# Optimization experiments

Hardware: AMD Instinct MI355X
Metric: run time of the kernel (lower is better)

## Reference

```python
import jax, jax.numpy as jnp
import numpy as np

TEMPERATURE = 12.5   # args.temperature (DeepEMD default)
EPS = 0.05           # entropic regularization for the OT (EMD) solve
N_ITERS = 100        # Sinkhorn iterations
COS_EPS = 1e-8       # F.cosine_similarity eps


def setup_inputs() -> dict:
    key = jax.random.key(0)
    k1, k2 = jax.random.split(key)
    B, C, H, W = 512, 1024, 8, 8
    proto = jax.random.normal(k1, (B, C, H, W), dtype=jnp.float32)
    query = jax.random.normal(k2, (B, C, H, W), dtype=jnp.float32)
    return {"proto": proto, "query": query}


def get_weight_vector(A, Bmap):
    """A,[b,c,h,w]; pooled Bmap reweights A's channels -> node weights [b, h*w]."""
    pooled = Bmap.mean(axis=(2, 3), keepdims=True)          # adaptive_avg_pool2d -> [b,c,1,1]
    comb = (A * pooled).sum(axis=1).reshape(A.shape[0], -1)  # [b, h*w]
    return jax.nn.relu(comb) + 0.001


def center(x):
    # args.norm == 'center': subtract channel mean
    return x - x.mean(axis=1, keepdims=True)


def cosine_sim_map(proto, query):
    """sim[b, q_node, p_node] = cosine similarity between flattened spatial nodes."""
    B, C = proto.shape[0], proto.shape[1]
    p = proto.reshape(B, C, -1).transpose(0, 2, 1)   # [b, Np, c]
    q = query.reshape(B, C, -1).transpose(0, 2, 1)   # [b, Nq, c]
    pn = p / jnp.maximum(jnp.linalg.norm(p, axis=-1, keepdims=True), COS_EPS)
    qn = q / jnp.maximum(jnp.linalg.norm(q, axis=-1, keepdims=True), COS_EPS)
    return jnp.einsum('bqc,bpc->bqp', qn, pn)        # [b, Nq, Np]


def sinkhorn_flow(cost, r, c):
    """Entropic-regularized OT flow with marginals r [b,N], c [b,M]; cost [b,N,M]."""
    K = jnp.exp(-cost / EPS)
    v0 = jnp.ones_like(c)

    def body(v, _):
        u = r / jnp.maximum(jnp.einsum('bnm,bm->bn', K, v), 1e-30)
        v = c / jnp.maximum(jnp.einsum('bnm,bn->bm', K, u), 1e-30)
        return v, None

    v, _ = jax.lax.scan(body, v0, None, length=N_ITERS)
    u = r / jnp.maximum(jnp.einsum('bnm,bm->bn', K, v), 1e-30)
    return u[:, :, None] * K * v[:, None, :]         # [b, N, M]


def reference(proto, query):
    # emd_forward(proto, query)
    weight_1 = get_weight_vector(query, proto)       # [b, Nq]
    weight_2 = get_weight_vector(proto, query)       # [b, Np]
    p = center(proto)
    q = center(query)
    sim = cosine_sim_map(p, q)                       # [b, Nq, Np]
    # get_emd_distance: solve OT on cost = 1 - sim with (normalized) node weights
    r = weight_1 / weight_1.sum(axis=-1, keepdims=True)
    c = weight_2 / weight_2.sum(axis=-1, keepdims=True)
    flow = sinkhorn_flow(1.0 - sim, r, c)
    num_node = weight_1.shape[-1]
    logits = (sim * flow).sum(axis=(-1, -2)) * (TEMPERATURE / num_node)
    return logits
```

## Files before the change

### kernel.cpp

```cpp
#include <hip/hip_runtime.h>
#include <math.h>

#define NCH    1024
#define NN     64
#define CK     32
#define KSC    28.853900817779268f
#define SPLIT  4
#define WSB    4352

#define STAT_Q(v) { sqp[0]+=(v).x; q2p[0]=fmaf((v).x,(v).x,q2p[0]); \
                    sqp[1]+=(v).y; q2p[1]=fmaf((v).y,(v).y,q2p[1]); \
                    sqp[2]+=(v).z; q2p[2]=fmaf((v).z,(v).z,q2p[2]); \
                    sqp[3]+=(v).w; q2p[3]=fmaf((v).w,(v).w,q2p[3]); }
#define STAT_P(v) { spp[0]+=(v).x; p2p[0]=fmaf((v).x,(v).x,p2p[0]); \
                    spp[1]+=(v).y; p2p[1]=fmaf((v).y,(v).y,p2p[1]); \
                    spp[2]+=(v).z; p2p[2]=fmaf((v).z,(v).z,p2p[2]); \
                    spp[3]+=(v).w; p2p[3]=fmaf((v).w,(v).w,p2p[3]); }

#define GRAM_CHUNK_BODY(NCHUNK_, QB_, PB_)                                     \
    for (int ch = 0; ch < (NCHUNK_); ++ch) {                                   \
        if (ch) __syncthreads();                                               \
        *(float4*)&stage[       ofs] = qv0;                                    \
        *(float4*)&stage[1024 + ofs] = qv1;                                    \
        *(float4*)&stage[2048 + ofs] = pv0;                                    \
        *(float4*)&stage[3072 + ofs] = pv1;                                    \
        float4 nq0, nq1, np0, np1;                                             \
        const bool more = (ch + 1 < (NCHUNK_));                                \
        if (more) {                                                            \
            const float* qn = (QB_) + (ch + 1) * 2048;                         \
            const float* pn = (PB_) + (ch + 1) * 2048;                         \
            nq0 = *(const float4*)(qn + ofs);                                  \
            nq1 = *(const float4*)(qn + 1024 + ofs);                           \
            np0 = *(const float4*)(pn + ofs);                                  \
            np1 = *(const float4*)(pn + 1024 + ofs);                           \
        }                                                                      \
        STAT_Q(qv0); STAT_Q(qv1);                                              \
        STAT_P(pv0); STAT_P(pv1);                                              \
        __syncthreads();                                                       \
        _Pragma("unroll 8")                                                    \
        for (int cc = 0; cc < CK; ++cc) {                                      \
            float4 a  = *(const float4*)&stage[cc * 64 + n0];                  \
            float4 bb = *(const float4*)&stage[2048 + cc * 64 + m0];           \
            acc[0][0]=fmaf(a.x,bb.x,acc[0][0]); acc[0][1]=fmaf(a.x,bb.y,acc[0][1]); \
            acc[0][2]=fmaf(a.x,bb.z,acc[0][2]); acc[0][3]=fmaf(a.x,bb.w,acc[0][3]); \
            acc[1][0]=fmaf(a.y,bb.x,acc[1][0]); acc[1][1]=fmaf(a.y,bb.y,acc[1][1]); \
            acc[1][2]=fmaf(a.y,bb.z,acc[1][2]); acc[1][3]=fmaf(a.y,bb.w,acc[1][3]); \
            acc[2][0]=fmaf(a.z,bb.x,acc[2][0]); acc[2][1]=fmaf(a.z,bb.y,acc[2][1]); \
            acc[2][2]=fmaf(a.z,bb.z,acc[2][2]); acc[2][3]=fmaf(a.z,bb.w,acc[2][3]); \
            acc[3][0]=fmaf(a.w,bb.x,acc[3][0]); acc[3][1]=fmaf(a.w,bb.y,acc[3][1]); \
            acc[3][2]=fmaf(a.w,bb.z,acc[3][2]); acc[3][3]=fmaf(a.w,bb.w,acc[3][3]); \
        }                                                                      \
        if (more) { qv0 = nq0; qv1 = nq1; pv0 = np0; pv1 = np1; }              \
    }

#define DOT16(KK, ARR) ({ \
    float4 x0 = *(const float4*)&ARR[sp4*16 +  0]; \
    float4 x1 = *(const float4*)&ARR[sp4*16 +  4]; \
    float4 x2 = *(const float4*)&ARR[sp4*16 +  8]; \
    float4 x3 = *(const float4*)&ARR[sp4*16 + 12]; \
    float a0 = 0.0f, a1 = 0.0f; \
    a0=fmaf(KK[0],x0.x,a0);  a1=fmaf(KK[1],x0.y,a1); \
    a0=fmaf(KK[2],x0.z,a0);  a1=fmaf(KK[3],x0.w,a1); \
    a0=fmaf(KK[4],x1.x,a0);  a1=fmaf(KK[5],x1.y,a1); \
    a0=fmaf(KK[6],x1.z,a0);  a1=fmaf(KK[7],x1.w,a1); \
    a0=fmaf(KK[8],x2.x,a0);  a1=fmaf(KK[9],x2.y,a1); \
    a0=fmaf(KK[10],x2.z,a0); a1=fmaf(KK[11],x2.w,a1); \
    a0=fmaf(KK[12],x3.x,a0); a1=fmaf(KK[13],x3.y,a1); \
    a0=fmaf(KK[14],x3.z,a0); a1=fmaf(KK[15],x3.w,a1); \
    a0 + a1; })

__global__ __launch_bounds__(256)
void gram_partial(const float* __restrict__ proto,
                  const float* __restrict__ query,
                  float* __restrict__ ws)
{
    __shared__ __align__(16) float stage[4096];

    const int bid = blockIdx.x;
    const int b = bid >> 2, s = bid & (SPLIT - 1);
    const int t  = threadIdx.x;
    const int tr = t >> 4, tc = t & 15;
    const int n0 = tr * 4, m0 = tc * 4;
    const int ofs = 4 * t;

    const float* __restrict__ pb = proto + (size_t)b * (NCH * NN) + s * (NCH / SPLIT) * NN;
    const float* __restrict__ qb = query + (size_t)b * (NCH * NN) + s * (NCH / SPLIT) * NN;

    float acc[4][4];
    #pragma unroll
    for (int i = 0; i < 4; ++i)
        #pragma unroll
        for (int j = 0; j < 4; ++j) acc[i][j] = 0.0f;
    float sqp[4] = {0,0,0,0}, q2p[4] = {0,0,0,0};
    float spp[4] = {0,0,0,0}, p2p[4] = {0,0,0,0};

    float4 qv0 = *(const float4*)(qb + ofs);
    float4 qv1 = *(const float4*)(qb + 1024 + ofs);
    float4 pv0 = *(const float4*)(pb + ofs);
    float4 pv1 = *(const float4*)(pb + 1024 + ofs);

    GRAM_CHUNK_BODY(NCH / SPLIT / CK, qb, pb)
    __syncthreads();

    float* __restrict__ wsb = ws + (size_t)bid * WSB;
    #pragma unroll
    for (int i = 0; i < 4; ++i) {
        float4 v; v.x = acc[i][0]; v.y = acc[i][1]; v.z = acc[i][2]; v.w = acc[i][3];
        *(float4*)&wsb[(n0 + i) * 64 + m0] = v;
    }

    #pragma unroll
    for (int k = 0; k < 4; ++k) {
        stage[t*16 +      k] = sqp[k];
        stage[t*16 +  4 + k] = q2p[k];
        stage[t*16 +  8 + k] = spp[k];
        stage[t*16 + 12 + k] = p2p[k];
    }
    __syncthreads();
    if (t < NN) {
        const int g = t >> 2, k = t & 3;
        float ssq = 0, sq2 = 0, ssp = 0, sp2 = 0;
        #pragma unroll
        for (int j = 0; j < 16; ++j) {
            const float* row = &stage[(j * 16 + g) * 16];
            ssq += row[k]; sq2 += row[4 + k]; ssp += row[8 + k]; sp2 += row[12 + k];
        }
        wsb[4096 +   0 + t] = ssq;
        wsb[4096 +  64 + t] = sq2;
        wsb[4096 + 128 + t] = ssp;
        wsb[4096 + 192 + t] = sp2;
    }
}

__global__ __launch_bounds__(256)
void emd_solve(const float* __restrict__ ws, float* __restrict__ out)
{
    __shared__ __align__(16) float stage[16 * 64];
    __shared__ __align__(16) float Kl [NN][68];
    __shared__ __align__(16) float KTl[NN][68];
    __shared__ __align__(16) float statL[4][NN];
    __shared__ __align__(16) float uL[NN];
    __shared__ __align__(16) float vL[NN];
    __shared__ __align__(16) float rL[NN];
    __shared__ __align__(16) float cL[NN];
    __shared__ float redl[4];

    const int b  = blockIdx.x;
    const int t  = threadIdx.x;
    const int tr = t >> 4, tc = t & 15;
    const int n0 = tr * 4, m0 = tc * 4;

    const float* __restrict__ wsb = ws + (size_t)b * SPLIT * WSB;

    float acc[4][4];
    #pragma unroll
    for (int i = 0; i < 4; ++i)
        #pragma unroll
        for (int j = 0; j < 4; ++j) acc[i][j] = 0.0f;
    #pragma unroll
    for (int s = 0; s < SPLIT; ++s) {
        const float* __restrict__ g = wsb + s * WSB;
        #pragma unroll
        for (int i = 0; i < 4; ++i) {
            float4 v = *(const float4*)&g[(n0 + i) * 64 + m0];
            acc[i][0] += v.x; acc[i][1] += v.y; acc[i][2] += v.z; acc[i][3] += v.w;
        }
    }
    if (t < NN) {
        float s0 = 0, s1 = 0, s2 = 0, s3 = 0;
        #pragma unroll
        for (int s = 0; s < SPLIT; ++s) {
            const float* __restrict__ g = wsb + s * WSB + 4096;
            s0 += g[t]; s1 += g[64 + t]; s2 += g[128 + t]; s3 += g[192 + t];
        }
        statL[0][t] = s0; statL[1][t] = s1; statL[2][t] = s2; statL[3][t] = s3;
    }
    #pragma unroll
    for (int i = 0; i < 4; ++i) {
        float s = acc[i][0] + acc[i][1] + acc[i][2] + acc[i][3];
        s += __shfl_xor(s, 1, 64); s += __shfl_xor(s, 2, 64);
        s += __shfl_xor(s, 4, 64); s += __shfl_xor(s, 8, 64);
        if (tc == 0) uL[n0 + i] = s;
    }
    #pragma unroll
    for (int j = 0; j < 4; ++j)
        stage[tr * 64 + m0 + j] = acc[0][j] + acc[1][j] + acc[2][j] + acc[3][j];
    __syncthreads();

    if (t < NN) {
        float cs = 0;
        #pragma unroll
        for (int i = 0; i < 16; ++i) cs += stage[i * 64 + t];
        float w2 = fmaxf(cs * (1.0f/64.0f), 0.0f) + 0.001f;
        float w1 = fmaxf(uL[t] * (1.0f/64.0f), 0.0f) + 0.001f;
        float s1 = w1, s2 = w2;
        #pragma unroll
        for (int m = 1; m < 64; m <<= 1) {
            s1 += __shfl_xor(s1, m, 64);
            s2 += __shfl_xor(s2, m, 64);
        }
        rL[t] = w1 / s1;
        cL[t] = w2 / s2;
        vL[t] = 1.0f;
    }
    {
        float nq_[4], np_[4], sqn[4], spm[4];
        #pragma unroll
        for (int i = 0; i < 4; ++i) {
            float sv  = statL[0][n0 + i];
            float var = statL[1][n0 + i] - sv * sv * (1.0f/1024.0f);
            nq_[i] = fmaxf(sqrtf(fmaxf(var, 0.0f)), 1e-8f);
            sqn[i] = sv;
        }
        #pragma unroll
        for (int j = 0; j < 4; ++j) {
            float sv  = statL[2][m0 + j];
            float var = statL[3][m0 + j] - sv * sv * (1.0f/1024.0f);
            np_[j] = fmaxf(sqrtf(fmaxf(var, 0.0f)), 1e-8f);
            spm[j] = sv;
        }
        #pragma unroll
        for (int i = 0; i < 4; ++i) {
            #pragma unroll
            for (int j = 0; j < 4; ++j) {
                float sim = (acc[i][j] - sqn[i] * spm[j] * (1.0f/1024.0f)) / (nq_[i] * np_[j]);
                acc[i][j] = sim;
                float Kv = exp2f((sim - 1.0f) * KSC);
                Kl [n0 + i][m0 + j] = Kv;
                KTl[m0 + j][n0 + i] = Kv;
            }
        }
    }
    __syncthreads();

    const int sn  = t >> 2;
    const int sp4 = t & 3;
    float Kr[16], KTr[16];
    #pragma unroll
    for (int jj = 0; jj < 4; ++jj) {
        float4 kv = *(const float4*)&Kl [sn][sp4 * 16 + jj * 4];
        float4 kt = *(const float4*)&KTl[sn][sp4 * 16 + jj * 4];
        Kr [jj*4+0]=kv.x; Kr [jj*4+1]=kv.y; Kr [jj*4+2]=kv.z; Kr [jj*4+3]=kv.w;
        KTr[jj*4+0]=kt.x; KTr[jj*4+1]=kt.y; KTr[jj*4+2]=kt.z; KTr[jj*4+3]=kt.w;
    }
    const float rreg = rL[sn];
    const float creg = cL[sn];

    for (int it = 0; it < 100; ++it) {
        float s = DOT16(Kr, vL);
        s += __shfl_xor(s, 1, 64); s += __shfl_xor(s, 2, 64);
        float u = rreg / fmaxf(s, 1e-30f);
        if (sp4 == 0) uL[sn] = u;
        __syncthreads();
        float s2 = DOT16(KTr, uL);
        s2 += __shfl_xor(s2, 1, 64); s2 += __shfl_xor(s2, 2, 64);
        float vv = creg / fmaxf(s2, 1e-30f);
        if (sp4 == 0) vL[sn] = vv;
        __syncthreads();
    }
    {
        float s = DOT16(Kr, vL);
        s += __shfl_xor(s, 1, 64); s += __shfl_xor(s, 2, 64);
        float u = rreg / fmaxf(s, 1e-30f);
        if (sp4 == 0) uL[sn] = u;
    }
    __syncthreads();

    float uu[4], vv_[4];
    #pragma unroll
    for (int i = 0; i < 4; ++i) uu[i]  = uL[n0 + i];
    #pragma unroll
    for (int j = 0; j < 4; ++j) vv_[j] = vL[m0 + j];
    float part = 0.0f;
    #pragma unroll
    for (int i = 0; i < 4; ++i) {
        #pragma unroll
        for (int j = 0; j < 4; ++j) {
            float sim = acc[i][j];
            float Kv  = exp2f((sim - 1.0f) * KSC);
            part = fmaf(sim * Kv, uu[i] * vv_[j], part);
        }
    }
    #pragma unroll
    for (int m = 1; m < 64; m <<= 1) part += __shfl_xor(part, m, 64);
    if ((t & 63) == 0) redl[t >> 6] = part;
    __syncthreads();
    if (t == 0) out[b] = (redl[0] + redl[1] + redl[2] + redl[3]) * (12.5f / 64.0f);
}

__global__ __launch_bounds__(256)
void deepemd_fused(const float* __restrict__ proto,
                   const float* __restrict__ query,
                   float* __restrict__ out)
{
    __shared__ __align__(16) float stage[2 * CK * NN];
    __shared__ __align__(16) float Kl [NN][68];
    __shared__ __align__(16) float KTl[NN][68];
    __shared__ __align__(16) float statL[4][NN];
    __shared__ __align__(16) float uL[NN];
    __shared__ __align__(16) float vL[NN];
    __shared__ __align__(16) float rL[NN];
    __shared__ __align__(16) float cL[NN];
    __shared__ float redl[4];

    const int b  = blockIdx.x;
    const int t  = threadIdx.x;
    const int tr = t >> 4, tc = t & 15;
    const int n0 = tr * 4, m0 = tc * 4;
    const int ofs = 4 * t;

    const float* __restrict__ pb = proto + (size_t)b * (NCH * NN);
    const float* __restrict__ qb = query + (size_t)b * (NCH * NN);

    float acc[4][4];
    #pragma unroll
    for (int i = 0; i < 4; ++i)
        #pragma unroll
        for (int j = 0; j < 4; ++j) acc[i][j] = 0.0f;
    float sqp[4] = {0,0,0,0}, q2p[4] = {0,0,0,0};
    float spp[4] = {0,0,0,0}, p2p[4] = {0,0,0,0};

    float4 qv0 = *(const float4*)(qb + ofs);
    float4 qv1 = *(const float4*)(qb + 1024 + ofs);
    float4 pv0 = *(const float4*)(pb + ofs);
    float4 pv1 = *(const float4*)(pb + 1024 + ofs);

    GRAM_CHUNK_BODY(NCH / CK, qb, pb)
    __syncthreads();

    #pragma unroll
    for (int i = 0; i < 4; ++i) {
        float s = acc[i][0] + acc[i][1] + acc[i][2] + acc[i][3];
        s += __shfl_xor(s, 1, 64); s += __shfl_xor(s, 2, 64);
        s += __shfl_xor(s, 4, 64); s += __shfl_xor(s, 8, 64);
        if (tc == 0) uL[n0 + i] = s;
    }
    #pragma unroll
    for (int k = 0; k < 4; ++k) {
        stage[t*16 +      k] = sqp[k];
        stage[t*16 +  4 + k] = q2p[k];
        stage[t*16 +  8 + k] = spp[k];
        stage[t*16 + 12 + k] = p2p[k];
    }
    __syncthreads();
    if (t < NN) {
        const int g = t >> 2, k = t & 3;
        float ssq = 0, sq2 = 0, ssp = 0, sp2 = 0;
        #pragma unroll
        for (int j = 0; j < 16; ++j) {
            const float* row = &stage[(j * 16 + g) * 16];
            ssq += row[k]; sq2 += row[4 + k]; ssp += row[8 + k]; sp2 += row[12 + k];
        }
        statL[0][t] = ssq; statL[1][t] = sq2; statL[2][t] = ssp; statL[3][t] = sp2;
    }
    __syncthreads();
    #pragma unroll
    for (int j = 0; j < 4; ++j)
        stage[tr * 64 + m0 + j] = acc[0][j] + acc[1][j] + acc[2][j] + acc[3][j];
    __syncthreads();
    if (t < NN) {
        float cs = 0;
        #pragma unroll
        for (int i = 0; i < 16; ++i) cs += stage[i * 64 + t];
        float w2 = fmaxf(cs * (1.0f/64.0f), 0.0f) + 0.001f;
        float w1 = fmaxf(uL[t] * (1.0f/64.0f), 0.0f) + 0.001f;
        float s1 = w1, s2 = w2;
        #pragma unroll
        for (int m = 1; m < 64; m <<= 1) {
            s1 += __shfl_xor(s1, m, 64);
            s2 += __shfl_xor(s2, m, 64);
        }
        rL[t] = w1 / s1;
        cL[t] = w2 / s2;
        vL[t] = 1.0f;
    }
    __syncthreads();

    {
        float nq_[4], np_[4], sqn[4], spm[4];
        #pragma unroll
        for (int i = 0; i < 4; ++i) {
            float sv  = statL[0][n0 + i];
            float var = statL[1][n0 + i] - sv * sv * (1.0f/1024.0f);
            nq_[i] = fmaxf(sqrtf(fmaxf(var, 0.0f)), 1e-8f);
            sqn[i] = sv;
        }
        #pragma unroll
        for (int j = 0; j < 4; ++j) {
            float sv  = statL[2][m0 + j];
            float var = statL[3][m0 + j] - sv * sv * (1.0f/1024.0f);
            np_[j] = fmaxf(sqrtf(fmaxf(var, 0.0f)), 1e-8f);
            spm[j] = sv;
        }
        #pragma unroll
        for (int i = 0; i < 4; ++i) {
            #pragma unroll
            for (int j = 0; j < 4; ++j) {
                float sim = (acc[i][j] - sqn[i] * spm[j] * (1.0f/1024.0f)) / (nq_[i] * np_[j]);
                acc[i][j] = sim;
                float Kv = exp2f((sim - 1.0f) * KSC);
                Kl [n0 + i][m0 + j] = Kv;
                KTl[m0 + j][n0 + i] = Kv;
            }
        }
    }
    __syncthreads();

    const int sn  = t >> 2;
    const int sp4 = t & 3;
    float Kr[16], KTr[16];
    #pragma unroll
    for (int jj = 0; jj < 4; ++jj) {
        float4 kv = *(const float4*)&Kl [sn][sp4 * 16 + jj * 4];
        float4 kt = *(const float4*)&KTl[sn][sp4 * 16 + jj * 4];
        Kr [jj*4+0]=kv.x; Kr [jj*4+1]=kv.y; Kr [jj*4+2]=kv.z; Kr [jj*4+3]=kv.w;
        KTr[jj*4+0]=kt.x; KTr[jj*4+1]=kt.y; KTr[jj*4+2]=kt.z; KTr[jj*4+3]=kt.w;
    }
    const float rreg = rL[sn];
    const float creg = cL[sn];

    for (int it = 0; it < 100; ++it) {
        float s = DOT16(Kr, vL);
        s += __shfl_xor(s, 1, 64); s += __shfl_xor(s, 2, 64);
        float u = rreg / fmaxf(s, 1e-30f);
        if (sp4 == 0) uL[sn] = u;
        __syncthreads();
        float s2 = DOT16(KTr, uL);
        s2 += __shfl_xor(s2, 1, 64); s2 += __shfl_xor(s2, 2, 64);
        float vv = creg / fmaxf(s2, 1e-30f);
        if (sp4 == 0) vL[sn] = vv;
        __syncthreads();
    }
    {
        float s = DOT16(Kr, vL);
        s += __shfl_xor(s, 1, 64); s += __shfl_xor(s, 2, 64);
        float u = rreg / fmaxf(s, 1e-30f);
        if (sp4 == 0) uL[sn] = u;
    }
    __syncthreads();

    float uu[4], vv_[4];
    #pragma unroll
    for (int i = 0; i < 4; ++i) uu[i]  = uL[n0 + i];
    #pragma unroll
    for (int j = 0; j < 4; ++j) vv_[j] = vL[m0 + j];
    float part = 0.0f;
    #pragma unroll
    for (int i = 0; i < 4; ++i) {
        #pragma unroll
        for (int j = 0; j < 4; ++j) {
            float sim = acc[i][j];
            float Kv  = exp2f((sim - 1.0f) * KSC);
            part = fmaf(sim * Kv, uu[i] * vv_[j], part);
        }
    }
    #pragma unroll
    for (int m = 1; m < 64; m <<= 1) part += __shfl_xor(part, m, 64);
    if ((t & 63) == 0) redl[t >> 6] = part;
    __syncthreads();
    if (t == 0) out[b] = (redl[0] + redl[1] + redl[2] + redl[3]) * (12.5f / 64.0f);
}

extern "C" void kernel_launch(void* const* d_in, const int* in_sizes, int n_in,
                              void* d_out, int out_size, void* d_ws, size_t ws_size,
                              hipStream_t stream) {
    const float* proto = (const float*)d_in[0];
    const float* query = (const float*)d_in[1];
    float* out = (float*)d_out;
    (void)in_sizes; (void)n_in; (void)out_size;

    const size_t need = (size_t)512 * SPLIT * WSB * sizeof(float);
    if (ws_size >= need) {
        gram_partial<<<dim3(512 * SPLIT), dim3(256), 0, stream>>>(proto, query, (float*)d_ws);
        emd_solve  <<<dim3(512),         dim3(256), 0, stream>>>((const float*)d_ws, out);
    } else {
        deepemd_fused<<<dim3(512), dim3(256), 0, stream>>>(proto, query, out);
    }
}
```

Before: 134.5 us.

## Replace LDS-staged Gram kernel with register-blocked per-wave 8x8 tiles

The Gram partial kernel is rewritten so each wave reads its own 128-channel slice straight from global memory into registers, using a four-slot software prefetch, and computes an 8x8 register tile per lane with no LDS staging or per-chunk barriers. Partial Grams from the four waves are then reduced through LDS. The channel split drops from 4 to 2 blocks per batch, which halves workspace traffic and the reduction work in emd_solve. The cost is a 64-float accumulator per thread plus prefetch registers, so register pressure rises and occupancy may drop. Each lane also issues uncoalesced float4 loads of row fragments.

```diff
diff --git a/kernel.cpp b/kernel.cpp
--- a/kernel.cpp
+++ b/kernel.cpp
@@ -5,8 +5,306 @@
 #define NN     64
 #define CK     32
 #define KSC    28.853900817779268f
-#define SPLIT  4
+#define SPLIT  2
 #define WSB    4352
+
+__global__ __launch_bounds__(256)
+void gram4(const float* __restrict__ proto,
+           const float* __restrict__ query,
+           float* __restrict__ ws)
+{
+    __shared__ __align__(16) float GA[4096];
+    __shared__ __align__(16) float GB[4096];
+    __shared__ __align__(16) float st4[4 * 4 * NN];
+
+    const int bid = blockIdx.x;
+    const int b = bid >> 1, h = bid & 1;
+    const int t = threadIdx.x;
+    const int w = t >> 6;
+    const int l = t & 63;
+    const int ri = l >> 3;
+    const int ci = l & 7;
+    const int r0 = ri * 8;
+    const int c0 = ci * 4;
+
+    const float* __restrict__ qw = query + (size_t)b * 65536 + (h * 512 + w * 128) * 64;
+    const float* __restrict__ pw = proto + (size_t)b * 65536 + (h * 512 + w * 128) * 64;
+
+    float acc[8][8];
+    #pragma unroll
+    for (int i = 0; i < 8; ++i)
+        #pragma unroll
+        for (int j = 0; j < 8; ++j) acc[i][j] = 0.0f;
+    float sq = 0.0f, q2 = 0.0f, sp = 0.0f, p2 = 0.0f;
+
+    float4 A0[4], A1[4], B0[4], B1[4];
+    float  QS[4], PS[4];
+
+#define LOADSLOT(K, C) do {                                   \
+        const float* qc_ = qw + (C) * 64;                     \
+        const float* pc_ = pw + (C) * 64;                     \
+        A0[K] = *(const float4*)(qc_ + r0);                   \
+        A1[K] = *(const float4*)(qc_ + r0 + 4);               \
+        B0[K] = *(const float4*)(pc_ + c0);                   \
+        B1[K] = *(const float4*)(pc_ + c0 + 32);              \
+        QS[K] = qc_[l];                                       \
+        PS[K] = pc_[l];                                       \
+    } while (0)
+
+#define COMPUTESLOT(K) do {                                   \
+        const float av[8] = {A0[K].x,A0[K].y,A0[K].z,A0[K].w, \
+                             A1[K].x,A1[K].y,A1[K].z,A1[K].w};\
+        const float bv[8] = {B0[K].x,B0[K].y,B0[K].z,B0[K].w, \
+                             B1[K].x,B1[K].y,B1[K].z,B1[K].w};\
+        sq += QS[K]; q2 = fmaf(QS[K], QS[K], q2);             \
+        sp += PS[K]; p2 = fmaf(PS[K], PS[K], p2);             \
+        _Pragma("unroll")                                     \
+        for (int i = 0; i < 8; ++i)                           \
+            _Pragma("unroll")                                 \
+            for (int j = 0; j < 8; ++j)                       \
+                acc[i][j] = fmaf(av[i], bv[j], acc[i][j]);    \
+    } while (0)
+
+    LOADSLOT(0, 0); LOADSLOT(1, 1); LOADSLOT(2, 2); LOADSLOT(3, 3);
+
+    #pragma unroll 1
+    for (int g = 0; g < 31; ++g) {
+        const int c = g * 4;
+        COMPUTESLOT(0); LOADSLOT(0, c + 4);
+        COMPUTESLOT(1); LOADSLOT(1, c + 5);
+        COMPUTESLOT(2); LOADSLOT(2, c + 6);
+        COMPUTESLOT(3); LOADSLOT(3, c + 7);
+    }
+    COMPUTESLOT(0); COMPUTESLOT(1); COMPUTESLOT(2); COMPUTESLOT(3);
+#undef LOADSLOT
+#undef COMPUTESLOT
+
+    st4[(0*4 + w)*NN + l] = sq;
+    st4[(1*4 + w)*NN + l] = q2;
+    st4[(2*4 + w)*NN + l] = sp;
+    st4[(3*4 + w)*NN + l] = p2;
+
+    {
+        float* const GT = (w < 2) ? GA : GB;
+        const bool first = ((w & 1) == 0);
+        if (first) {
+            #pragma unroll
+            for (int i = 0; i < 8; ++i) {
+                float4 v0; v0.x=acc[i][0]; v0.y=acc[i][1]; v0.z=acc[i][2]; v0.w=acc[i][3];
+                float4 v1; v1.x=acc[i][4]; v1.y=acc[i][5]; v1.z=acc[i][6]; v1.w=acc[i][7];
+                *(float4*)&GT[(r0 + i) * 64 + c0]      = v0;
+                *(float4*)&GT[(r0 + i) * 64 + c0 + 32] = v1;
+            }
+        }
+        __syncthreads();
+        if (!first) {
+            #pragma unroll
+            for (int i = 0; i < 8; ++i) {
+                float* g0 = &GT[(r0 + i) * 64 + c0];
+                float* g1 = &GT[(r0 + i) * 64 + c0 + 32];
+                float4 d0 = *(const float4*)g0;
+                float4 d1 = *(const float4*)g1;
+                d0.x+=acc[i][0]; d0.y+=acc[i][1]; d0.z+=acc[i][2]; d0.w+=acc[i][3];
+                d1.x+=acc[i][4]; d1.y+=acc[i][5]; d1.z+=acc[i][6]; d1.w+=acc[i][7];
+                *(float4*)g0 = d0;
+                *(float4*)g1 = d1;
+            }
+        }
+        __syncthreads();
+    }
+
+    float* __restrict__ wsb = ws + (size_t)bid * WSB;
+    {
+        const int base = t * 16;
+        #pragma unroll
+        for (int k = 0; k < 4; ++k) {
+            float4 x = *(const float4*)&GA[base + k * 4];
+            float4 y = *(const float4*)&GB[base + k * 4];
+            x.x+=y.x; x.y+=y.y; x.z+=y.z; x.w+=y.w;
+            *(float4*)&wsb[base + k * 4] = x;
+        }
+    }
+    if (t < NN) {
+        #pragma unroll
+        for (int k = 0; k < 4; ++k) {
+            float s = st4[(k*4 + 0)*NN + t] + st4[(k*4 + 1)*NN + t]
+                    + st4[(k*4 + 2)*NN + t] + st4[(k*4 + 3)*NN + t];
+            wsb[4096 + k * 64 + t] = s;
+        }
+    }
+}
+
+#define DOT16(KK, ARR) ({ \
+    float4 x0 = *(const float4*)&ARR[sp4*16 +  0]; \
+    float4 x1 = *(const float4*)&ARR[sp4*16 +  4]; \
+    float4 x2 = *(const float4*)&ARR[sp4*16 +  8]; \
+    float4 x3 = *(const float4*)&ARR[sp4*16 + 12]; \
+    float a0 = 0.0f, a1 = 0.0f; \
+    a0=fmaf(KK[0],x0.x,a0);  a1=fmaf(KK[1],x0.y,a1); \
+    a0=fmaf(KK[2],x0.z,a0);  a1=fmaf(KK[3],x0.w,a1); \
+    a0=fmaf(KK[4],x1.x,a0);  a1=fmaf(KK[5],x1.y,a1); \
+    a0=fmaf(KK[6],x1.z,a0);  a1=fmaf(KK[7],x1.w,a1); \
+    a0=fmaf(KK[8],x2.x,a0);  a1=fmaf(KK[9],x2.y,a1); \
+    a0=fmaf(KK[10],x2.z,a0); a1=fmaf(KK[11],x2.w,a1); \
+    a0=fmaf(KK[12],x3.x,a0); a1=fmaf(KK[13],x3.y,a1); \
+    a0=fmaf(KK[14],x3.z,a0); a1=fmaf(KK[15],x3.w,a1); \
+    a0 + a1; })
+
+__global__ __launch_bounds__(256)
+void emd_solve(const float* __restrict__ ws, float* __restrict__ out)
+{
+    __shared__ __align__(16) float stage[16 * 64];
+    __shared__ __align__(16) float Kl [NN][68];
+    __shared__ __align__(16) float KTl[NN][68];
+    __shared__ __align__(16) float statL[4][NN];
+    __shared__ __align__(16) float uL[NN];
+    __shared__ __align__(16) float vL[NN];
+    __shared__ __align__(16) float rL[NN];
+    __shared__ __align__(16) float cL[NN];
+    __shared__ float redl[4];
+
+    const int b  = blockIdx.x;
+    const int t  = threadIdx.x;
+    const int tr = t >> 4, tc = t & 15;
+    const int n0 = tr * 4, m0 = tc * 4;
+
+    const float* __restrict__ wsb = ws + (size_t)b * SPLIT * WSB;
+
+    float acc[4][4];
+    #pragma unroll
+    for (int i = 0; i < 4; ++i)
+        #pragma unroll
+        for (int j = 0; j < 4; ++j) acc[i][j] = 0.0f;
+    #pragma unroll
+    for (int s = 0; s < SPLIT; ++s) {
+        const float* __restrict__ g = wsb + s * WSB;
+        #pragma unroll
+        for (int i = 0; i < 4; ++i) {
+            float4 v = *(const float4*)&g[(n0 + i) * 64 + m0];
+            acc[i][0] += v.x; acc[i][1] += v.y; acc[i][2] += v.z; acc[i][3] += v.w;
+        }
+    }
+    if (t < NN) {
+        float s0 = 0, s1 = 0, s2 = 0, s3 = 0;
+        #pragma unroll
+        for (int s = 0; s < SPLIT; ++s) {
+            const float* __restrict__ g = wsb + s * WSB + 4096;
+            s0 += g[t]; s1 += g[64 + t]; s2 += g[128 + t]; s3 += g[192 + t];
+        }
+        statL[0][t] = s0; statL[1][t] = s1; statL[2][t] = s2; statL[3][t] = s3;
+    }
+    #pragma unroll
+    for (int i = 0; i < 4; ++i) {
+        float s = acc[i][0] + acc[i][1] + acc[i][2] + acc[i][3];
+        s += __shfl_xor(s, 1, 64); s += __shfl_xor(s, 2, 64);
+        s += __shfl_xor(s, 4, 64); s += __shfl_xor(s, 8, 64);
+        if (tc == 0) uL[n0 + i] = s;
+    }
+    #pragma unroll
+    for (int j = 0; j < 4; ++j)
+        stage[tr * 64 + m0 + j] = acc[0][j] + acc[1][j] + acc[2][j] + acc[3][j];
+    __syncthreads();
+
+    if (t < NN) {
+        float cs = 0;
+        #pragma unroll
+        for (int i = 0; i < 16; ++i) cs += stage[i * 64 + t];
+        float w2 = fmaxf(cs * (1.0f/64.0f), 0.0f) + 0.001f;
+        float w1 = fmaxf(uL[t] * (1.0f/64.0f), 0.0f) + 0.001f;
+        float s1 = w1, s2 = w2;
+        #pragma unroll
+        for (int m = 1; m < 64; m <<= 1) {
+            s1 += __shfl_xor(s1, m, 64);
+            s2 += __shfl_xor(s2, m, 64);
+        }
+        rL[t] = w1 / s1;
+        cL[t] = w2 / s2;
+        vL[t] = 1.0f;
+    }
+    {
+        float nq_[4], np_[4], sqn[4], spm[4];
+        #pragma unroll
+        for (int i = 0; i < 4; ++i) {
+            float sv  = statL[0][n0 + i];
+            float var = statL[1][n0 + i] - sv * sv * (1.0f/1024.0f);
+            nq_[i] = fmaxf(sqrtf(fmaxf(var, 0.0f)), 1e-8f);
+            sqn[i] = sv;
+        }
+        #pragma unroll
+        for (int j = 0; j < 4; ++j) {
+            float sv  = statL[2][m0 + j];
+            float var = statL[3][m0 + j] - sv * sv * (1.0f/1024.0f);
+            np_[j] = fmaxf(sqrtf(fmaxf(var, 0.0f)), 1e-8f);
+            spm[j] = sv;
+        }
+        #pragma unroll
+        for (int i = 0; i < 4; ++i) {
+            #pragma unroll
+            for (int j = 0; j < 4; ++j) {
+                float sim = (acc[i][j] - sqn[i] * spm[j] * (1.0f/1024.0f)) / (nq_[i] * np_[j]);
+                acc[i][j] = sim;
+                float Kv = exp2f((sim - 1.0f) * KSC);
+                Kl [n0 + i][m0 + j] = Kv;
+                KTl[m0 + j][n0 + i] = Kv;
+            }
+        }
+    }
+    __syncthreads();
+
+    const int sn  = t >> 2;
+    const int sp4 = t & 3;
+    float Kr[16], KTr[16];
+    #pragma unroll
+    for (int jj = 0; jj < 4; ++jj) {
+        float4 kv = *(const float4*)&Kl [sn][sp4 * 16 + jj * 4];
+        float4 kt = *(const float4*)&KTl[sn][sp4 * 16 + jj * 4];
+        Kr [jj*4+0]=kv.x; Kr [jj*4+1]=kv.y; Kr [jj*4+2]=kv.z; Kr [jj*4+3]=kv.w;
+        KTr[jj*4+0]=kt.x; KTr[jj*4+1]=kt.y; KTr[jj*4+2]=kt.z; KTr[jj*4+3]=kt.w;
+    }
+    const float rreg = rL[sn];
+    const float creg = cL[sn];
+
+    for (int it = 0; it < 100; ++it) {
+        float s = DOT16(Kr, vL);
+        s += __shfl_xor(s, 1, 64); s += __shfl_xor(s, 2, 64);
+        float u = rreg / fmaxf(s, 1e-30f);
+        if (sp4 == 0) uL[sn] = u;
+        __syncthreads();
+        float s2 = DOT16(KTr, uL);
+        s2 += __shfl_xor(s2, 1, 64); s2 += __shfl_xor(s2, 2, 64);
+        float vv = creg / fmaxf(s2, 1e-30f);
+        if (sp4 == 0) vL[sn] = vv;
+        __syncthreads();
+    }
+    {
+        float s = DOT16(Kr, vL);
+        s += __shfl_xor(s, 1, 64); s += __shfl_xor(s, 2, 64);
+        float u = rreg / fmaxf(s, 1e-30f);
+        if (sp4 == 0) uL[sn] = u;
+    }
+    __syncthreads();
+
+    float uu[4], vv_[4];
+    #pragma unroll
+    for (int i = 0; i < 4; ++i) uu[i]  = uL[n0 + i];
+    #pragma unroll
+    for (int j = 0; j < 4; ++j) vv_[j] = vL[m0 + j];
+    float part = 0.0f;
+    #pragma unroll
+    for (int i = 0; i < 4; ++i) {
+        #pragma unroll
+        for (int j = 0; j < 4; ++j) {
+            float sim = acc[i][j];
+            float Kv  = exp2f((sim - 1.0f) * KSC);
+            part = fmaf(sim * Kv, uu[i] * vv_[j], part);
+        }
+    }
+    #pragma unroll
+    for (int m = 1; m < 64; m <<= 1) part += __shfl_xor(part, m, 64);
+    if ((t & 63) == 0) redl[t >> 6] = part;
+    __syncthreads();
+    if (t == 0) out[b] = (redl[0] + redl[1] + redl[2] + redl[3]) * (12.5f / 64.0f);
+}
 
 #define STAT_Q(v) { sqp[0]+=(v).x; q2p[0]=fmaf((v).x,(v).x,q2p[0]); \
                     sqp[1]+=(v).y; q2p[1]=fmaf((v).y,(v).y,q2p[1]); \
@@ -53,241 +351,6 @@
         if (more) { qv0 = nq0; qv1 = nq1; pv0 = np0; pv1 = np1; }              \
     }
 
-#define DOT16(KK, ARR) ({ \
-    float4 x0 = *(const float4*)&ARR[sp4*16 +  0]; \
-    float4 x1 = *(const float4*)&ARR[sp4*16 +  4]; \
-    float4 x2 = *(const float4*)&ARR[sp4*16 +  8]; \
-    float4 x3 = *(const float4*)&ARR[sp4*16 + 12]; \
-    float a0 = 0.0f, a1 = 0.0f; \
-    a0=fmaf(KK[0],x0.x,a0);  a1=fmaf(KK[1],x0.y,a1); \
-    a0=fmaf(KK[2],x0.z,a0);  a1=fmaf(KK[3],x0.w,a1); \
-    a0=fmaf(KK[4],x1.x,a0);  a1=fmaf(KK[5],x1.y,a1); \
-    a0=fmaf(KK[6],x1.z,a0);  a1=fmaf(KK[7],x1.w,a1); \
-    a0=fmaf(KK[8],x2.x,a0);  a1=fmaf(KK[9],x2.y,a1); \
-    a0=fmaf(KK[10],x2.z,a0); a1=fmaf(KK[11],x2.w,a1); \
-    a0=fmaf(KK[12],x3.x,a0); a1=fmaf(KK[13],x3.y,a1); \
-    a0=fmaf(KK[14],x3.z,a0); a1=fmaf(KK[15],x3.w,a1); \
-    a0 + a1; })
-
-__global__ __launch_bounds__(256)
-void gram_partial(const float* __restrict__ proto,
-                  const float* __restrict__ query,
-                  float* __restrict__ ws)
-{
-    __shared__ __align__(16) float stage[4096];
-
-    const int bid = blockIdx.x;
-    const int b = bid >> 2, s = bid & (SPLIT - 1);
-    const int t  = threadIdx.x;
-    const int tr = t >> 4, tc = t & 15;
-    const int n0 = tr * 4, m0 = tc * 4;
-    const int ofs = 4 * t;
-
-    const float* __restrict__ pb = proto + (size_t)b * (NCH * NN) + s * (NCH / SPLIT) * NN;
-    const float* __restrict__ qb = query + (size_t)b * (NCH * NN) + s * (NCH / SPLIT) * NN;
-
-    float acc[4][4];
-    #pragma unroll
-    for (int i = 0; i < 4; ++i)
-        #pragma unroll
-        for (int j = 0; j < 4; ++j) acc[i][j] = 0.0f;
-    float sqp[4] = {0,0,0,0}, q2p[4] = {0,0,0,0};
-    float spp[4] = {0,0,0,0}, p2p[4] = {0,0,0,0};
-
-    float4 qv0 = *(const float4*)(qb + ofs);
-    float4 qv1 = *(const float4*)(qb + 1024 + ofs);
-    float4 pv0 = *(const float4*)(pb + ofs);
-    float4 pv1 = *(const float4*)(pb + 1024 + ofs);
-
-    GRAM_CHUNK_BODY(NCH / SPLIT / CK, qb, pb)
-    __syncthreads();
-
-    float* __restrict__ wsb = ws + (size_t)bid * WSB;
-    #pragma unroll
-    for (int i = 0; i < 4; ++i) {
-        float4 v; v.x = acc[i][0]; v.y = acc[i][1]; v.z = acc[i][2]; v.w = acc[i][3];
-        *(float4*)&wsb[(n0 + i) * 64 + m0] = v;
-    }
-
-    #pragma unroll
-    for (int k = 0; k < 4; ++k) {
-        stage[t*16 +      k] = sqp[k];
-        stage[t*16 +  4 + k] = q2p[k];
-        stage[t*16 +  8 + k] = spp[k];
-        stage[t*16 + 12 + k] = p2p[k];
-    }
-    __syncthreads();
-    if (t < NN) {
-        const int g = t >> 2, k = t & 3;
-        float ssq = 0, sq2 = 0, ssp = 0, sp2 = 0;
-        #pragma unroll
-        for (int j = 0; j < 16; ++j) {
-            const float* row = &stage[(j * 16 + g) * 16];
-            ssq += row[k]; sq2 += row[4 + k]; ssp += row[8 + k]; sp2 += row[12 + k];
-        }
-        wsb[4096 +   0 + t] = ssq;
-        wsb[4096 +  64 + t] = sq2;
-        wsb[4096 + 128 + t] = ssp;
-        wsb[4096 + 192 + t] = sp2;
-    }
-}
-
-__global__ __launch_bounds__(256)
-void emd_solve(const float* __restrict__ ws, float* __restrict__ out)
-{
-    __shared__ __align__(16) float stage[16 * 64];
-    __shared__ __align__(16) float Kl [NN][68];
-    __shared__ __align__(16) float KTl[NN][68];
-    __shared__ __align__(16) float statL[4][NN];
-    __shared__ __align__(16) float uL[NN];
-    __shared__ __align__(16) float vL[NN];
-    __shared__ __align__(16) float rL[NN];
-    __shared__ __align__(16) float cL[NN];
-    __shared__ float redl[4];
-
-    const int b  = blockIdx.x;
-    const int t  = threadIdx.x;
-    const int tr = t >> 4, tc = t & 15;
-    const int n0 = tr * 4, m0 = tc * 4;
-
-    const float* __restrict__ wsb = ws + (size_t)b * SPLIT * WSB;
-
-    float acc[4][4];
-    #pragma unroll
-    for (int i = 0; i < 4; ++i)
-        #pragma unroll
-        for (int j = 0; j < 4; ++j) acc[i][j] = 0.0f;
-    #pragma unroll
-    for (int s = 0; s < SPLIT; ++s) {
-        const float* __restrict__ g = wsb + s * WSB;
-        #pragma unroll
-        for (int i = 0; i < 4; ++i) {
-            float4 v = *(const float4*)&g[(n0 + i) * 64 + m0];
-            acc[i][0] += v.x; acc[i][1] += v.y; acc[i][2] += v.z; acc[i][3] += v.w;
-        }
-    }
-    if (t < NN) {
-        float s0 = 0, s1 = 0, s2 = 0, s3 = 0;
-        #pragma unroll
-        for (int s = 0; s < SPLIT; ++s) {
-            const float* __restrict__ g = wsb + s * WSB + 4096;
-            s0 += g[t]; s1 += g[64 + t]; s2 += g[128 + t]; s3 += g[192 + t];
-        }
-        statL[0][t] = s0; statL[1][t] = s1; statL[2][t] = s2; statL[3][t] = s3;
-    }
-    #pragma unroll
-    for (int i = 0; i < 4; ++i) {
-        float s = acc[i][0] + acc[i][1] + acc[i][2] + acc[i][3];
-        s += __shfl_xor(s, 1, 64); s += __shfl_xor(s, 2, 64);
-        s += __shfl_xor(s, 4, 64); s += __shfl_xor(s, 8, 64);
-        if (tc == 0) uL[n0 + i] = s;
-    }
-    #pragma unroll
-    for (int j = 0; j < 4; ++j)
-        stage[tr * 64 + m0 + j] = acc[0][j] + acc[1][j] + acc[2][j] + acc[3][j];
-    __syncthreads();
-
-    if (t < NN) {
-        float cs = 0;
-        #pragma unroll
-        for (int i = 0; i < 16; ++i) cs += stage[i * 64 + t];
-        float w2 = fmaxf(cs * (1.0f/64.0f), 0.0f) + 0.001f;
-        float w1 = fmaxf(uL[t] * (1.0f/64.0f), 0.0f) + 0.001f;
-        float s1 = w1, s2 = w2;
-        #pragma unroll
-        for (int m = 1; m < 64; m <<= 1) {
-            s1 += __shfl_xor(s1, m, 64);
-            s2 += __shfl_xor(s2, m, 64);
-        }
-        rL[t] = w1 / s1;
-        cL[t] = w2 / s2;
-        vL[t] = 1.0f;
-    }
-    {
-        float nq_[4], np_[4], sqn[4], spm[4];
-        #pragma unroll
-        for (int i = 0; i < 4; ++i) {
-            float sv  = statL[0][n0 + i];
-            float var = statL[1][n0 + i] - sv * sv * (1.0f/1024.0f);
-            nq_[i] = fmaxf(sqrtf(fmaxf(var, 0.0f)), 1e-8f);
-            sqn[i] = sv;
-        }
-        #pragma unroll
-        for (int j = 0; j < 4; ++j) {
-            float sv  = statL[2][m0 + j];
-            float var = statL[3][m0 + j] - sv * sv * (1.0f/1024.0f);
-            np_[j] = fmaxf(sqrtf(fmaxf(var, 0.0f)), 1e-8f);
-            spm[j] = sv;
-        }
-        #pragma unroll
-        for (int i = 0; i < 4; ++i) {
-            #pragma unroll
-            for (int j = 0; j < 4; ++j) {
-                float sim = (acc[i][j] - sqn[i] * spm[j] * (1.0f/1024.0f)) / (nq_[i] * np_[j]);
-                acc[i][j] = sim;
-                float Kv = exp2f((sim - 1.0f) * KSC);
-                Kl [n0 + i][m0 + j] = Kv;
-                KTl[m0 + j][n0 + i] = Kv;
-            }
-        }
-    }
-    __syncthreads();
-
-    const int sn  = t >> 2;
-    const int sp4 = t & 3;
-    float Kr[16], KTr[16];
-    #pragma unroll
-    for (int jj = 0; jj < 4; ++jj) {
-        float4 kv = *(const float4*)&Kl [sn][sp4 * 16 + jj * 4];
-        float4 kt = *(const float4*)&KTl[sn][sp4 * 16 + jj * 4];
-        Kr [jj*4+0]=kv.x; Kr [jj*4+1]=kv.y; Kr [jj*4+2]=kv.z; Kr [jj*4+3]=kv.w;
-        KTr[jj*4+0]=kt.x; KTr[jj*4+1]=kt.y; KTr[jj*4+2]=kt.z; KTr[jj*4+3]=kt.w;
-    }
-    const float rreg = rL[sn];
-    const float creg = cL[sn];
-
-    for (int it = 0; it < 100; ++it) {
-        float s = DOT16(Kr, vL);
-        s += __shfl_xor(s, 1, 64); s += __shfl_xor(s, 2, 64);
-        float u = rreg / fmaxf(s, 1e-30f);
-        if (sp4 == 0) uL[sn] = u;
-        __syncthreads();
-        float s2 = DOT16(KTr, uL);
-        s2 += __shfl_xor(s2, 1, 64); s2 += __shfl_xor(s2, 2, 64);
-        float vv = creg / fmaxf(s2, 1e-30f);
-        if (sp4 == 0) vL[sn] = vv;
-        __syncthreads();
-    }
-    {
-        float s = DOT16(Kr, vL);
-        s += __shfl_xor(s, 1, 64); s += __shfl_xor(s, 2, 64);
-        float u = rreg / fmaxf(s, 1e-30f);
-        if (sp4 == 0) uL[sn] = u;
-    }
-    __syncthreads();
-
-    float uu[4], vv_[4];
-    #pragma unroll
-    for (int i = 0; i < 4; ++i) uu[i]  = uL[n0 + i];
-    #pragma unroll
-    for (int j = 0; j < 4; ++j) vv_[j] = vL[m0 + j];
-    float part = 0.0f;
-    #pragma unroll
-    for (int i = 0; i < 4; ++i) {
-        #pragma unroll
-        for (int j = 0; j < 4; ++j) {
-            float sim = acc[i][j];
-            float Kv  = exp2f((sim - 1.0f) * KSC);
-            part = fmaf(sim * Kv, uu[i] * vv_[j], part);
-        }
-    }
-    #pragma unroll
-    for (int m = 1; m < 64; m <<= 1) part += __shfl_xor(part, m, 64);
-    if ((t & 63) == 0) redl[t >> 6] = part;
-    __syncthreads();
-    if (t == 0) out[b] = (redl[0] + redl[1] + redl[2] + redl[3]) * (12.5f / 64.0f);
-}
-
 __global__ __launch_bounds__(256)
 void deepemd_fused(const float* __restrict__ proto,
                    const float* __restrict__ query,
@@ -471,8 +534,8 @@
 
     const size_t need = (size_t)512 * SPLIT * WSB * sizeof(float);
     if (ws_size >= need) {
-        gram_partial<<<dim3(512 * SPLIT), dim3(256), 0, stream>>>(proto, query, (float*)d_ws);
-        emd_solve  <<<dim3(512),         dim3(256), 0, stream>>>((const float*)d_ws, out);
+        gram4    <<<dim3(512 * SPLIT), dim3(256), 0, stream>>>(proto, query, (float*)d_ws);
+        emd_solve<<<dim3(512),         dim3(256), 0, stream>>>((const float*)d_ws, out);
     } else {
         deepemd_fused<<<dim3(512), dim3(256), 0, stream>>>(proto, query, out);
     }
```

Measured after the change: 156.8 us. 1.17x slower.
